# Optimization experiments

Hardware: AMD Instinct MI355X
Metric: run time of the kernel (lower is better)

The kernel has to match this reference:

```python
import jax, jax.numpy as jnp
import numpy as np

N0 = 50000
N1 = 50000
E = 500000
IN_DIM = 128
OUT_DIM = 128
H = 8
DK = OUT_DIM // H  # 16
SQRT_DK = float(np.sqrt(DK))
NUM_TYPES = 2
NUM_REL = 3
# relations: (src_type, dst_type, e_id)
RELATIONS = [(0, 1, 0), (1, 0, 1), (0, 0, 2)]


def setup_inputs() -> dict:
    key = jax.random.key(0)
    ks = jax.random.split(key, 24)
    d = {}
    d["h0"] = jax.random.normal(ks[0], (N0, IN_DIM), dtype=jnp.float32)
    d["h1"] = jax.random.normal(ks[1], (N1, IN_DIM), dtype=jnp.float32)
    d["src0"] = jax.random.randint(ks[2], (E,), 0, N0)
    d["dst0"] = jax.random.randint(ks[3], (E,), 0, N1)
    d["src1"] = jax.random.randint(ks[4], (E,), 0, N1)
    d["dst1"] = jax.random.randint(ks[5], (E,), 0, N0)
    d["src2"] = jax.random.randint(ks[6], (E,), 0, N0)
    d["dst2"] = jax.random.randint(ks[7], (E,), 0, N0)
    w_scale = 1.0 / np.sqrt(IN_DIM)
    # per-node-type stacked linear weights (k, q, v, a), torch Linear convention: y = x @ W.T + b
    d["Wk"] = jax.random.normal(ks[8], (NUM_TYPES, OUT_DIM, IN_DIM), dtype=jnp.float32) * w_scale
    d["bk"] = jnp.zeros((NUM_TYPES, OUT_DIM), dtype=jnp.float32)
    d["Wq"] = jax.random.normal(ks[9], (NUM_TYPES, OUT_DIM, IN_DIM), dtype=jnp.float32) * w_scale
    d["bq"] = jnp.zeros((NUM_TYPES, OUT_DIM), dtype=jnp.float32)
    d["Wv"] = jax.random.normal(ks[10], (NUM_TYPES, OUT_DIM, IN_DIM), dtype=jnp.float32) * w_scale
    d["bv"] = jnp.zeros((NUM_TYPES, OUT_DIM), dtype=jnp.float32)
    d["Wa"] = jax.random.normal(ks[11], (NUM_TYPES, OUT_DIM, OUT_DIM), dtype=jnp.float32) * w_scale
    d["ba"] = jnp.zeros((NUM_TYPES, OUT_DIM), dtype=jnp.float32)
    xavier = float(np.sqrt(6.0 / (DK + DK)))
    d["rel_att"] = jax.random.uniform(ks[12], (NUM_REL, H, DK, DK), dtype=jnp.float32, minval=-xavier, maxval=xavier)
    d["rel_msg"] = jax.random.uniform(ks[13], (NUM_REL, H, DK, DK), dtype=jnp.float32, minval=-xavier, maxval=xavier)
    d["rel_pri"] = jnp.ones((NUM_REL, H), dtype=jnp.float32)
    d["skip"] = jnp.ones((NUM_TYPES,), dtype=jnp.float32)
    return d


def _lin(x, W, b):
    return x @ W.T + b


def reference(h0, h1, src0, dst0, src1, dst1, src2, dst2,
              Wk, bk, Wq, bq, Wv, bv, Wa, ba,
              rel_att, rel_msg, rel_pri, skip):
    h = [h0, h1]
    edges = [(src0, dst0), (src1, dst1), (src2, dst2)]
    # per-type projections, reshaped to (N, H, DK)
    k = [_lin(h[t], Wk[t], bk[t]).reshape(-1, H, DK) for t in range(NUM_TYPES)]
    q = [_lin(h[t], Wq[t], bq[t]).reshape(-1, H, DK) for t in range(NUM_TYPES)]
    v = [_lin(h[t], Wv[t], bv[t]).reshape(-1, H, DK) for t in range(NUM_TYPES)]

    agg = [[] for _ in range(NUM_TYPES)]
    for (s, dt, e), (src, dst) in zip(RELATIONS, edges):
        # relation-specific transforms of source k and v
        kr = jnp.einsum('nhi,hij->nhj', k[s], rel_att[e])
        vr = jnp.einsum('nhi,hij->nhj', v[s], rel_msg[e])
        # per-edge dot-product score (E, H)
        score = (q[dt][dst] * kr[src]).sum(-1) * rel_pri[e] / SQRT_DK
        n_dst = h[dt].shape[0]
        # edge softmax normalized by dst (stable)
        m = jax.ops.segment_max(score, dst, num_segments=n_dst)
        ex = jnp.exp(score - m[dst])
        den = jax.ops.segment_sum(ex, dst, num_segments=n_dst)
        attn = ex / den[dst]  # (E, H)
        # weighted message scatter-sum -> (n_dst, H, DK)
        msg = vr[src] * attn[:, :, None]
        agg[dt].append(jax.ops.segment_sum(msg, dst, num_segments=n_dst))

    new_h = []
    for t in range(NUM_TYPES):
        # cross_reducer='mean' over relations targeting this node type
        tmean = sum(agg[t]) / float(len(agg[t]))
        tflat = tmean.reshape(-1, OUT_DIM)
        trans = _lin(tflat, Wa[t], ba[t])  # dropout = identity (eval)
        alpha = jax.nn.sigmoid(skip[t])
        new_h.append(trans * alpha + h[t] * (1.0 - alpha))
    return tuple(new_h)
```

## Files before the change

### kernel.cpp

```cpp
#include <hip/hip_runtime.h>

typedef __attribute__((ext_vector_type(8))) short bf16x8;
typedef __attribute__((ext_vector_type(4))) float f32x4;

#define NB 196
#define CHK 2048
#define CAPB 4096
#define PSTRIDE 6144

__device__ __forceinline__ float bflo(unsigned u) { return __uint_as_float(u << 16); }
__device__ __forceinline__ float bfhi(unsigned u) { return __uint_as_float(u & 0xFFFF0000u); }
__device__ __forceinline__ unsigned f2bf(float f) {
  unsigned u = __float_as_uint(f);
  u = (u + 0x7FFFu + ((u >> 16) & 1u)) >> 16;
  return u;
}

__global__ void cvt2_kernel(const float* __restrict__ a, unsigned short* __restrict__ oa,
                            const float* __restrict__ b, unsigned short* __restrict__ ob,
                            int n8) {
  int i = blockIdx.x * 256 + threadIdx.x;
  if (i >= n8) return;
  const float* in = blockIdx.y ? b : a;
  unsigned short* out = blockIdx.y ? ob : oa;
  const float4* p = (const float4*)(in + (size_t)i * 8);
  float4 x = p[0], y = p[1];
  uint4 v;
  v.x = f2bf(x.x) | (f2bf(x.y) << 16);
  v.y = f2bf(x.z) | (f2bf(x.w) << 16);
  v.z = f2bf(y.x) | (f2bf(y.y) << 16);
  v.w = f2bf(y.z) | (f2bf(y.w) << 16);
  *(uint4*)(out + (size_t)i * 8) = v;
}

__global__ void compose_w_kernel(const float* __restrict__ Wk, const float* __restrict__ bk,
                                 const float* __restrict__ Wv, const float* __restrict__ bv,
                                 const float* __restrict__ rel_att, const float* __restrict__ rel_msg,
                                 const float* __restrict__ rel_pri,
                                 unsigned short* __restrict__ Wkr, float* __restrict__ bkr,
                                 unsigned short* __restrict__ Wvr, float* __restrict__ bvr) {
  int e = blockIdx.x;
  int o = blockIdx.y;
  int z = blockIdx.z;
  int c = threadIdx.x;
  int hd = o >> 4, j = o & 15;
  const int se[3] = {0, 1, 0};
  int s = se[e];
  const float* W = z ? Wv : Wk;
  const float* b = z ? bv : bk;
  const float* R = z ? rel_msg : rel_att;
  float scale = z ? 1.0f : (rel_pri[e * 8 + hd] * 0.25f);
  float acc = 0.0f, bacc = 0.0f;
#pragma unroll
  for (int i = 0; i < 16; ++i) {
    float r = R[((e * 8 + hd) * 16 + i) * 16 + j];
    acc += W[(s * 128 + hd * 16 + i) * 128 + c] * r;
    bacc += b[s * 128 + hd * 16 + i] * r;
  }
  unsigned short* Wo = z ? Wvr : Wkr;
  float* bo = z ? bvr : bkr;
  Wo[((size_t)e * 128 + o) * 128 + c] = (unsigned short)f2bf(acc * scale);
  if (c == 0) bo[e * 128 + o] = bacc * scale;
}

struct ProjFP {
  const float* A[2];
  int M[2];
  int nj[2];
  const unsigned short* W[10];
  const float* b[10];
  unsigned short* out[10];
  int ostr[10];
};

__global__ __launch_bounds__(256) void proj_gemm_fused(ProjFP P) {
  __shared__ short As[128 * 128];
  __shared__ short Bs[128 * 128];
  int type = blockIdx.y;
  const float* __restrict__ A = P.A[type];
  int M = P.M[type];
  int nj = P.nj[type];
  int base = type * 5;
  int row0 = blockIdx.x * 128;
  if (row0 >= M) return;
  int t = threadIdx.x;
  bool full = (row0 + 128 <= M);
#pragma unroll
  for (int it = 0; it < 8; ++it) {
    int o = (it * 256 + t) * 8;
    int row = o >> 7, col = o & 127;
    int gr = row0 + row;
    uint4 av = make_uint4(0, 0, 0, 0);
    if (full || gr < M) {
      float4 x = *(const float4*)(A + (size_t)gr * 128 + col);
      float4 y = *(const float4*)(A + (size_t)gr * 128 + col + 4);
      av.x = f2bf(x.x) | (f2bf(x.y) << 16);
      av.y = f2bf(x.z) | (f2bf(x.w) << 16);
      av.z = f2bf(y.x) | (f2bf(y.y) << 16);
      av.w = f2bf(y.z) | (f2bf(y.w) << 16);
    }
    int sw = o ^ ((row & 7) << 3);
    *(uint4*)(&As[sw]) = av;
  }
  {
    const unsigned short* W0 = P.W[base];
#pragma unroll
    for (int it = 0; it < 8; ++it) {
      int o = (it * 256 + t) * 8;
      int row = o >> 7;
      int sw = o ^ ((row & 7) << 3);
      *(uint4*)(&Bs[sw]) = *(const uint4*)(W0 + o);
    }
  }
  __syncthreads();
  int wid = t >> 6, l = t & 63;
  int wr = wid >> 1, wc = wid & 1;
  int lr = l & 15, kb = l >> 4;
  for (int j = 0;; ++j) {
    f32x4 acc[4][4] = {};
#pragma unroll
    for (int ks = 0; ks < 4; ++ks) {
      bf16x8 af[4], bfr[4];
#pragma unroll
      for (int m = 0; m < 4; ++m) {
        int row = wr * 64 + m * 16 + lr;
        int h = (row * 128 + kb * 8 + ks * 32) ^ ((row & 7) << 3);
        af[m] = *(bf16x8*)(&As[h]);
      }
#pragma unroll
      for (int n = 0; n < 4; ++n) {
        int row = wc * 64 + n * 16 + lr;
        int h = (row * 128 + kb * 8 + ks * 32) ^ ((row & 7) << 3);
        bfr[n] = *(bf16x8*)(&Bs[h]);
      }
#pragma unroll
      for (int m = 0; m < 4; ++m)
#pragma unroll
        for (int n = 0; n < 4; ++n)
          acc[m][n] = __builtin_amdgcn_mfma_f32_16x16x32_bf16(af[m], bfr[n], acc[m][n], 0, 0, 0);
    }
    const float* bias = P.b[base + j];
    unsigned short* out = P.out[base + j];
    int ostr = P.ostr[base + j];
    int rb = row0 + wr * 64 + (l >> 4) * 4;
#pragma unroll
    for (int m = 0; m < 4; ++m)
#pragma unroll
      for (int jr = 0; jr < 4; ++jr) {
        int grow = rb + m * 16 + jr;
        if (grow < M) {
#pragma unroll
          for (int n = 0; n < 4; ++n) {
            int col = wc * 64 + n * 16 + lr;
            out[(size_t)grow * ostr + col] = (unsigned short)f2bf(acc[m][n][jr] + bias[col]);
          }
        }
      }
    if (j + 1 >= nj) break;
    __syncthreads();
    {
      const unsigned short* Wj = P.W[base + j + 1];
#pragma unroll
      for (int it = 0; it < 8; ++it) {
        int o = (it * 256 + t) * 8;
        int row = o >> 7;
        int sw = o ^ ((row & 7) << 3);
        *(uint4*)(&Bs[sw]) = *(const uint4*)(Wj + o);
      }
    }
    __syncthreads();
  }
}

__global__ __launch_bounds__(256) void final_gemm_mfma(
    float* __restrict__ dout, const unsigned short* __restrict__ Tb0,
    const unsigned short* __restrict__ Tb1, const unsigned short* __restrict__ Wab,
    const float* __restrict__ ba, const float* __restrict__ h0, const float* __restrict__ h1,
    const float* __restrict__ skip, int N0, int N1) {
  __shared__ short As[128 * 128];
  __shared__ short Bs[128 * 128];
  int type = blockIdx.y;
  int M = type ? N1 : N0;
  const unsigned short* T = type ? Tb1 : Tb0;
  const unsigned short* W = Wab + (size_t)type * 16384;
  const float* bias = ba + type * 128;
  const float* h = type ? h1 : h0;
  float* O = dout + (type ? (size_t)N0 * 128 : 0);
  int row0 = blockIdx.x * 128;
  if (row0 >= M) return;
  int t = threadIdx.x;
  bool full = (row0 + 128 <= M);
#pragma unroll
  for (int it = 0; it < 8; ++it) {
    int o = (it * 256 + t) * 8;
    int row = o >> 7;
    int gr = row0 + row;
    uint4 av = make_uint4(0, 0, 0, 0);
    if (full || gr < M) av = *(const uint4*)(T + (size_t)gr * 128 + (o & 127));
    int sw = o ^ ((row & 7) << 3);
    *(uint4*)(&As[sw]) = av;
    uint4 wv = *(const uint4*)(W + o);
    *(uint4*)(&Bs[sw]) = wv;
  }
  __syncthreads();
  int wid = t >> 6, l = t & 63;
  int wr = wid >> 1, wc = wid & 1;
  int lr = l & 15, kb = l >> 4;
  f32x4 acc[4][4] = {};
#pragma unroll
  for (int ks = 0; ks < 4; ++ks) {
    bf16x8 af[4], bfr[4];
#pragma unroll
    for (int m = 0; m < 4; ++m) {
      int row = wr * 64 + m * 16 + lr;
      int h2 = (row * 128 + kb * 8 + ks * 32) ^ ((row & 7) << 3);
      af[m] = *(bf16x8*)(&As[h2]);
    }
#pragma unroll
    for (int n = 0; n < 4; ++n) {
      int row = wc * 64 + n * 16 + lr;
      int h2 = (row * 128 + kb * 8 + ks * 32) ^ ((row & 7) << 3);
      bfr[n] = *(bf16x8*)(&Bs[h2]);
    }
#pragma unroll
    for (int m = 0; m < 4; ++m)
#pragma unroll
      for (int n = 0; n < 4; ++n)
        acc[m][n] = __builtin_amdgcn_mfma_f32_16x16x32_bf16(af[m], bfr[n], acc[m][n], 0, 0, 0);
  }
  float alpha = 1.0f / (1.0f + __expf(-skip[type]));
  float beta = 1.0f - alpha;
  int rb = row0 + wr * 64 + (l >> 4) * 4;
#pragma unroll
  for (int m = 0; m < 4; ++m)
#pragma unroll
    for (int jr = 0; jr < 4; ++jr) {
      int grow = rb + m * 16 + jr;
      if (grow < M) {
#pragma unroll
        for (int n = 0; n < 4; ++n) {
          int col = wc * 64 + n * 16 + lr;
          float vout = alpha * (acc[m][n][jr] + bias[col]) + beta * h[(size_t)grow * 128 + col];
          O[(size_t)grow * 128 + col] = vout;
        }
      }
    }
}


__global__ __launch_bounds__(256) void bhist_kernel(const int* __restrict__ d0,
                                                    const int* __restrict__ d1,
                                                    const int* __restrict__ d2,
                                                    int* __restrict__ bh, int E) {
  __shared__ int lh[NB];
  int r = blockIdx.y;
  const int* dst = r == 0 ? d0 : (r == 1 ? d1 : d2);
  int t = threadIdx.x;
  int lo = blockIdx.x * CHK;
  int hi = lo + CHK < E ? lo + CHK : E;
  for (int j = t; j < NB; j += 256) lh[j] = 0;
  __syncthreads();
  for (int i = lo + t; i < hi; i += 256) atomicAdd(&lh[dst[i] >> 8], 1);
  __syncthreads();
  for (int j = t; j < NB; j += 256) {
    int v = lh[j];
    if (v) atomicAdd(&bh[r * NB + j], v);
  }
}

__global__ void bscan_kernel(const int* __restrict__ bh, int* __restrict__ bbase, int E) {
  __shared__ int sdm[256];
  int r = blockIdx.x;
  int t = threadIdx.x;
  int v = (t < NB) ? bh[r * NB + t] : 0;
  sdm[t] = v;
  __syncthreads();
  for (int off = 1; off < 256; off <<= 1) {
    int u = (t >= off) ? sdm[t - off] : 0;
    __syncthreads();
    sdm[t] += u;
    __syncthreads();
  }
  if (t < NB) bbase[r * (NB + 1) + t] = sdm[t] - v;
  if (t == 0) bbase[r * (NB + 1) + NB] = E;
}

__global__ __launch_bounds__(256) void bin_kernel(
    const int* __restrict__ s0, const int* __restrict__ d0, const int* __restrict__ s1,
    const int* __restrict__ d1, const int* __restrict__ s2, const int* __restrict__ d2,
    const int* __restrict__ bbase, int* __restrict__ bcur, unsigned* __restrict__ bo0,
    unsigned* __restrict__ bo1, unsigned* __restrict__ bo2, int E) {
  __shared__ unsigned st[CHK];
  __shared__ int ga[CHK];
  __shared__ int hist[NB];
  __shared__ int scn[256];
  __shared__ int gb[NB];
  int r = blockIdx.y;
  const int* src = r == 0 ? s0 : (r == 1 ? s1 : s2);
  const int* dst = r == 0 ? d0 : (r == 1 ? d1 : d2);
  unsigned* bo = r == 0 ? bo0 : (r == 1 ? bo1 : bo2);
  const int* bb = bbase + r * (NB + 1);
  int t = threadIdx.x;
  int lo = blockIdx.x * CHK;
  int hi = lo + CHK < E ? lo + CHK : E;
  int nloc = hi - lo;
  if (nloc <= 0) return;
  for (int j = t; j < NB; j += 256) hist[j] = 0;
  __syncthreads();
  int myb[CHK / 256], myr[CHK / 256];
  unsigned mye[CHK / 256];
#pragma unroll
  for (int k = 0; k < CHK / 256; ++k) {
    int i = lo + k * 256 + t;
    myb[k] = -1;
    if (i < hi) {
      int d = dst[i];
      int b = d >> 8;
      mye[k] = (unsigned)src[i] | ((unsigned)d << 16);
      myb[k] = b;
      myr[k] = atomicAdd(&hist[b], 1);
    }
  }
  __syncthreads();
  int v = (t < NB) ? hist[t] : 0;
  scn[t] = v;
  __syncthreads();
  for (int off = 1; off < 256; off <<= 1) {
    int u = (t >= off) ? scn[t - off] : 0;
    __syncthreads();
    scn[t] += u;
    __syncthreads();
  }
  int excl = scn[t] - v;
  __syncthreads();
  scn[t] = excl;
  if (t < NB && v > 0) gb[t] = atomicAdd(&bcur[r * NB + t], v);
  __syncthreads();
#pragma unroll
  for (int k = 0; k < CHK / 256; ++k) {
    if (myb[k] >= 0) {
      int slot = scn[myb[k]] + myr[k];
      st[slot] = mye[k];
      ga[slot] = bb[myb[k]] + gb[myb[k]] + myr[k];
    }
  }
  __syncthreads();
  for (int j = t; j < nloc; j += 256) bo[ga[j]] = st[j];
}

__global__ __launch_bounds__(256) void bsort_kernel(
    const unsigned* __restrict__ bo0, const unsigned* __restrict__ bo1,
    const unsigned* __restrict__ bo2, const int* __restrict__ bbase, int* __restrict__ rs0,
    int* __restrict__ rs1, int* __restrict__ rs2, int* __restrict__ re0, int* __restrict__ re1,
    int* __restrict__ re2, unsigned* __restrict__ sp0, unsigned* __restrict__ sp1,
    unsigned* __restrict__ sp2, int* __restrict__ bused, int nd0, int nd1, int nd2) {
  __shared__ unsigned ed[CAPB];
  __shared__ unsigned srt[PSTRIDE];
  __shared__ unsigned short rank[CAPB];
  __shared__ int hist[256];
  __shared__ int scn[256];
  int r = blockIdx.y, b = blockIdx.x;
  const unsigned* bo = r == 0 ? bo0 : (r == 1 ? bo1 : bo2);
  int* rs = r == 0 ? rs0 : (r == 1 ? rs1 : rs2);
  int* re = r == 0 ? re0 : (r == 1 ? re1 : re2);
  unsigned* sp = r == 0 ? sp0 : (r == 1 ? sp1 : sp2);
  int nd = r == 0 ? nd0 : (r == 1 ? nd1 : nd2);
  const int* bb = bbase + r * (NB + 1);
  int base = bb[b], endb = bb[b + 1];
  int cnt = endb - base;
  if (cnt > CAPB) cnt = CAPB;
  int nlo = b << 8;
  int nn = nd - nlo;
  if (nn > 256) nn = 256;
  if (nn < 0) nn = 0;
  int t = threadIdx.x;
  hist[t] = 0;
  for (int j = t; j < cnt; j += 256) ed[j] = bo[base + j];
  __syncthreads();
  for (int j = t; j < cnt; j += 256) {
    int node = (ed[j] >> 16) & 255;
    rank[j] = (unsigned short)atomicAdd(&hist[node], 1);
  }
  __syncthreads();
  int rawh = hist[t];
  int pd = (rawh + 7) & ~7;
  scn[t] = pd;
  __syncthreads();
  for (int off = 1; off < 256; off <<= 1) {
    int u = (t >= off) ? scn[t - off] : 0;
    __syncthreads();
    scn[t] += u;
    __syncthreads();
  }
  int pexcl = scn[t] - pd;
  int ptot = scn[255];
  __syncthreads();
  hist[t] = pexcl;
  __syncthreads();
  if (t < nn) {
    rs[nlo + t] = b * PSTRIDE + pexcl;
    re[nlo + t] = b * PSTRIDE + pexcl + pd;
  }
  int ptot32 = (ptot + 31) & ~31;
  for (int j = t; j < ptot32; j += 256) srt[j] = 0xFFFFFFFFu;
  __syncthreads();
  for (int j = t; j < cnt; j += 256) {
    int node = (ed[j] >> 16) & 255;
    srt[hist[node] + rank[j]] = ed[j];
  }
  __syncthreads();
  unsigned* spb = sp + (size_t)b * PSTRIDE;
  for (int j = t; j < ptot32; j += 256) spb[j] = srt[j];
  if (t == 0) bused[r * NB + b] = ptot32;
}

struct ScP {
  const unsigned* sp[3];
  const unsigned* kv[3];
  const unsigned* qb[3];
  unsigned short* eb[3];
  const int* bused;
  int ns[3];
  int ndv[3];
};

__global__ __launch_bounds__(256) void score_kernel(ScP P) {
  int r = blockIdx.y;
  int bx = blockIdx.x;
  int bucket = bx / (PSTRIDE / 32);
  int off = (bx % (PSTRIDE / 32)) * 32;
  int used = P.bused[r * NB + bucket];
  if (off >= used) return;
  const unsigned* __restrict__ sp = P.sp[r];
  const unsigned* __restrict__ kv = P.kv[r];
  const unsigned* __restrict__ qb = P.qb[r];
  unsigned short* __restrict__ eb = P.eb[r];
  unsigned smax = (unsigned)P.ns[r] - 1;
  unsigned dmax = (unsigned)P.ndv[r] - 1;
  int t = threadIdx.x;
  int p = bucket * PSTRIDE + off + (t >> 3);
  int h = t & 7;
  unsigned pk = sp[p];
  unsigned s = pk & 0xFFFFu;
  unsigned d = pk >> 16;
  unsigned sc2 = s > smax ? smax : s;
  unsigned dc = d > dmax ? dmax : d;
  const uint4* kr = (const uint4*)((const char*)kv + ((size_t)sc2 << 9) + h * 32);
  const uint4* qr = (const uint4*)((const char*)qb + ((size_t)dc << 8) + h * 32);
  uint4 k1 = kr[0], k2 = kr[1];
  uint4 q1 = qr[0], q2 = qr[1];
  float sc = 0.f;
#pragma unroll
  for (int c = 0; c < 4; ++c) {
    unsigned ku = ((const unsigned*)&k1)[c], qu = ((const unsigned*)&q1)[c];
    sc = fmaf(bflo(ku), bflo(qu), sc);
    sc = fmaf(bfhi(ku), bfhi(qu), sc);
  }
#pragma unroll
  for (int c = 0; c < 4; ++c) {
    unsigned ku = ((const unsigned*)&k2)[c], qu = ((const unsigned*)&q2)[c];
    sc = fmaf(bflo(ku), bflo(qu), sc);
    sc = fmaf(bfhi(ku), bfhi(qu), sc);
  }
  float e = (s == 0xFFFFu) ? 0.f : __expf(sc);
  eb[(size_t)(p & ~7) * 8 + h * 8 + (p & 7)] = (unsigned short)f2bf(e);
}

struct AgP {
  const unsigned *sp0, *sp1, *sp2;
  const unsigned short *eb0, *eb1, *eb2;
  const unsigned *kv0, *kv1, *kv2;
  const int *rs0, *rs1, *rs2;
  const int *re0, *re1, *re2;
  unsigned *Tb0, *Tb1;
  int ns0, ns1, ns2;
  int N0, N1;
};

__device__ __forceinline__ void loadV(const char* __restrict__ kvl,
                                      const unsigned* __restrict__ sp,
                                      const unsigned short* __restrict__ eb, int p,
                                      unsigned smax, int half, int h, uint2 vb[4], uint2& ev) {
  unsigned sv = sp[p + (threadIdx.x & 7)];
  ev = *(const uint2*)(eb + (size_t)p * 8 + h * 8 + half * 4);
#pragma unroll
  for (int g = 0; g < 4; ++g) {
    unsigned plo = __builtin_amdgcn_readlane(sv, g);
    unsigned phi = __builtin_amdgcn_readlane(sv, g + 4);
    unsigned pk = half ? phi : plo;
    unsigned s = pk & 0xFFFFu;
    s = s > smax ? smax : s;
    vb[g] = *(const uint2*)(kvl + ((size_t)s << 9));
  }
}

__device__ __forceinline__ void computeV(const uint2 vb[4], uint2 ev, float& a0, float& a1,
                                         float& a2, float& a3, float& den) {
  float eg[4] = {bflo(ev.x), bfhi(ev.x), bflo(ev.y), bfhi(ev.y)};
#pragma unroll
  for (int g = 0; g < 4; ++g) {
    float e = eg[g];
    den += e;
    a0 = fmaf(e, bflo(vb[g].x), a0);
    a1 = fmaf(e, bfhi(vb[g].x), a1);
    a2 = fmaf(e, bflo(vb[g].y), a2);
    a3 = fmaf(e, bfhi(vb[g].y), a3);
  }
}

__device__ __forceinline__ void agg_rel(const unsigned* __restrict__ sp,
                                        const unsigned short* __restrict__ eb,
                                        const unsigned* __restrict__ kv,
                                        const int* __restrict__ rs, const int* __restrict__ re,
                                        int node, int ll, int half, unsigned smax,
                                        float& r0, float& r1, float& r2, float& r3) {
  int beg = __builtin_amdgcn_readfirstlane(rs[node]);
  int end = __builtin_amdgcn_readfirstlane(re[node]);
  if (end <= beg) return;
  int h = ll >> 2;
  const char* kvl = (const char*)kv + 256 + ll * 8;
  float a0 = 0.f, a1 = 0.f, a2 = 0.f, a3 = 0.f, den = 0.f;
  uint2 va[4], vb[4];
  uint2 ea, ebv;
  int p = beg;
  loadV(kvl, sp, eb, p, smax, half, h, va, ea);
  for (;;) {
    if (p + 8 < end) loadV(kvl, sp, eb, p + 8, smax, half, h, vb, ebv);
    computeV(va, ea, a0, a1, a2, a3, den);
    p += 8;
    if (p >= end) break;
    if (p + 8 < end) loadV(kvl, sp, eb, p + 8, smax, half, h, va, ea);
    computeV(vb, ebv, a0, a1, a2, a3, den);
    p += 8;
    if (p >= end) break;
  }
  den += __shfl_xor(den, 32);
  a0 += __shfl_xor(a0, 32);
  a1 += __shfl_xor(a1, 32);
  a2 += __shfl_xor(a2, 32);
  a3 += __shfl_xor(a3, 32);
  float inv = 1.0f / den;
  r0 = fmaf(a0, inv, r0);
  r1 = fmaf(a1, inv, r1);
  r2 = fmaf(a2, inv, r2);
  r3 = fmaf(a3, inv, r3);
}

__global__ __launch_bounds__(256) void agg2_kernel(AgP P) {
  int gw = (blockIdx.x * 256 + threadIdx.x) >> 6;
  int l = threadIdx.x & 63;
  int ll = l & 31, half = l >> 5;
  if (gw < P.N0) {
    float r0 = 0.f, r1 = 0.f, r2 = 0.f, r3 = 0.f;
    agg_rel(P.sp1, P.eb1, P.kv1, P.rs1, P.re1, gw, ll, half, (unsigned)P.ns1 - 1, r0, r1, r2, r3);
    agg_rel(P.sp2, P.eb2, P.kv2, P.rs2, P.re2, gw, ll, half, (unsigned)P.ns2 - 1, r0, r1, r2, r3);
    if (half == 0) {
      uint2 o;
      o.x = f2bf(r0 * 0.5f) | (f2bf(r1 * 0.5f) << 16);
      o.y = f2bf(r2 * 0.5f) | (f2bf(r3 * 0.5f) << 16);
      *(uint2*)(P.Tb0 + (size_t)gw * 64 + 2 * ll) = o;
    }
  } else if (gw < P.N0 + P.N1) {
    int n = gw - P.N0;
    float r0 = 0.f, r1 = 0.f, r2 = 0.f, r3 = 0.f;
    agg_rel(P.sp0, P.eb0, P.kv0, P.rs0, P.re0, n, ll, half, (unsigned)P.ns0 - 1, r0, r1, r2, r3);
    if (half == 0) {
      uint2 o;
      o.x = f2bf(r0) | (f2bf(r1) << 16);
      o.y = f2bf(r2) | (f2bf(r3) << 16);
      *(uint2*)(P.Tb1 + (size_t)n * 64 + 2 * ll) = o;
    }
  }
}

extern "C" void kernel_launch(void* const* d_in, const int* in_sizes, int n_in,
                              void* d_out, int out_size, void* d_ws, size_t ws_size,
                              hipStream_t stream) {
  const float* h0 = (const float*)d_in[0];
  const float* h1 = (const float*)d_in[1];
  const int* srcs[3] = {(const int*)d_in[2], (const int*)d_in[4], (const int*)d_in[6]};
  const int* dsts[3] = {(const int*)d_in[3], (const int*)d_in[5], (const int*)d_in[7]};
  const float* Wk = (const float*)d_in[8];
  const float* bk = (const float*)d_in[9];
  const float* Wq = (const float*)d_in[10];
  const float* bq = (const float*)d_in[11];
  const float* Wv = (const float*)d_in[12];
  const float* bv = (const float*)d_in[13];
  const float* Wa = (const float*)d_in[14];
  const float* ba = (const float*)d_in[15];
  const float* rel_att = (const float*)d_in[16];
  const float* rel_msg = (const float*)d_in[17];
  const float* rel_pri = (const float*)d_in[18];
  const float* skip = (const float*)d_in[19];

  int N0 = in_sizes[0] / 128;
  int N1 = in_sizes[1] / 128;
  int E = in_sizes[2];
  int nsrc[3] = {N0, N1, N0};
  int ndst[3] = {N1, N0, N0};
  int maxN = N0 > N1 ? N0 : N1;

  char* base = (char*)d_ws;
  size_t off = 0;
  auto alloc = [&](size_t bytes) -> void* {
    void* p = base + off;
    off += (bytes + 255) & ~(size_t)255;
    return p;
  };

  unsigned short* qb0 = (unsigned short*)alloc((size_t)N0 * 128 * 2);
  unsigned short* qb1 = (unsigned short*)alloc((size_t)N1 * 128 * 2);
  unsigned short* kvb[3];
  for (int r = 0; r < 3; ++r) kvb[r] = (unsigned short*)alloc((size_t)nsrc[r] * 256 * 2);
  unsigned short* Tb0 = (unsigned short*)alloc((size_t)N0 * 128 * 2);
  unsigned short* Tb1 = (unsigned short*)alloc((size_t)N1 * 128 * 2);
  unsigned short* Wkrb = (unsigned short*)alloc((size_t)3 * 16384 * 2);
  unsigned short* Wvrb = (unsigned short*)alloc((size_t)3 * 16384 * 2);
  unsigned short* Wqb = (unsigned short*)alloc((size_t)2 * 16384 * 2);
  unsigned short* Wab = (unsigned short*)alloc((size_t)2 * 16384 * 2);
  float* bkr = (float*)alloc(3 * 128 * 4);
  float* bvr = (float*)alloc(3 * 128 * 4);
  int* rp_s[3];
  int* rp_e[3];
  unsigned* spk[3];
  unsigned short* eb[3];
  unsigned* bo[3];
  for (int r = 0; r < 3; ++r) {
    rp_s[r] = (int*)alloc((size_t)ndst[r] * 4);
    rp_e[r] = (int*)alloc((size_t)ndst[r] * 4);
    spk[r] = (unsigned*)alloc((size_t)NB * PSTRIDE * 4);
    eb[r] = (unsigned short*)alloc((size_t)NB * PSTRIDE * 8 * 2);
    bo[r] = (unsigned*)alloc((size_t)(E + 8) * 4);
  }
  int* bcnt = (int*)alloc((size_t)2 * 3 * NB * 4);
  int* bhist = bcnt;
  int* bcur = bcnt + 3 * NB;
  int* bbase = (int*)alloc((size_t)3 * (NB + 1) * 4);
  int* bused = (int*)alloc((size_t)3 * NB * 4);
  (void)ws_size;

  compose_w_kernel<<<dim3(3, 128, 2), 128, 0, stream>>>(Wk, bk, Wv, bv, rel_att, rel_msg,
                                                        rel_pri, Wkrb, bkr, Wvrb, bvr);
  cvt2_kernel<<<dim3(16, 2), 256, 0, stream>>>(Wq, Wqb, Wa, Wab, 4096);

  ProjFP pf;
  pf.A[0] = h0; pf.A[1] = h1;
  pf.M[0] = N0; pf.M[1] = N1;
  pf.nj[0] = 5; pf.nj[1] = 3;
  pf.W[0] = Wqb;            pf.b[0] = bq;        pf.out[0] = qb0;          pf.ostr[0] = 128;
  pf.W[1] = Wkrb;           pf.b[1] = bkr;       pf.out[1] = kvb[0];       pf.ostr[1] = 256;
  pf.W[2] = Wkrb + 32768;   pf.b[2] = bkr + 256; pf.out[2] = kvb[2];       pf.ostr[2] = 256;
  pf.W[3] = Wvrb;           pf.b[3] = bvr;       pf.out[3] = kvb[0] + 128; pf.ostr[3] = 256;
  pf.W[4] = Wvrb + 32768;   pf.b[4] = bvr + 256; pf.out[4] = kvb[2] + 128; pf.ostr[4] = 256;
  pf.W[5] = Wqb + 16384;    pf.b[5] = bq + 128;  pf.out[5] = qb1;          pf.ostr[5] = 128;
  pf.W[6] = Wkrb + 16384;   pf.b[6] = bkr + 128; pf.out[6] = kvb[1];       pf.ostr[6] = 256;
  pf.W[7] = Wvrb + 16384;   pf.b[7] = bvr + 128; pf.out[7] = kvb[1] + 128; pf.ostr[7] = 256;
  pf.W[8] = Wqb; pf.b[8] = bq; pf.out[8] = qb0; pf.ostr[8] = 128;
  pf.W[9] = Wqb; pf.b[9] = bq; pf.out[9] = qb0; pf.ostr[9] = 128;
  proj_gemm_fused<<<dim3((maxN + 127) / 128, 2), 256, 0, stream>>>(pf);

  hipMemsetAsync(bcnt, 0, (size_t)2 * 3 * NB * 4, stream);
  bhist_kernel<<<dim3((E + CHK - 1) / CHK, 3), 256, 0, stream>>>(dsts[0], dsts[1], dsts[2],
                                                                 bhist, E);
  bscan_kernel<<<3, 256, 0, stream>>>(bhist, bbase, E);
  bin_kernel<<<dim3((E + CHK - 1) / CHK, 3), 256, 0, stream>>>(
      srcs[0], dsts[0], srcs[1], dsts[1], srcs[2], dsts[2], bbase, bcur, bo[0], bo[1], bo[2], E);
  bsort_kernel<<<dim3(NB, 3), 256, 0, stream>>>(
      bo[0], bo[1], bo[2], bbase, rp_s[0], rp_s[1], rp_s[2], rp_e[0], rp_e[1], rp_e[2],
      spk[0], spk[1], spk[2], bused, ndst[0], ndst[1], ndst[2]);

  ScP sp;
  for (int r = 0; r < 3; ++r) {
    sp.sp[r] = spk[r];
    sp.kv[r] = (const unsigned*)kvb[r];
    sp.eb[r] = eb[r];
    sp.ns[r] = nsrc[r];
    sp.ndv[r] = ndst[r];
  }
  sp.bused = bused;
  sp.qb[0] = (const unsigned*)qb1;
  sp.qb[1] = (const unsigned*)qb0;
  sp.qb[2] = (const unsigned*)qb0;
  score_kernel<<<dim3(NB * (PSTRIDE / 32), 3), 256, 0, stream>>>(sp);

  AgP ap;
  ap.sp0 = spk[0]; ap.sp1 = spk[1]; ap.sp2 = spk[2];
  ap.eb0 = eb[0]; ap.eb1 = eb[1]; ap.eb2 = eb[2];
  ap.kv0 = (const unsigned*)kvb[0]; ap.kv1 = (const unsigned*)kvb[1];
  ap.kv2 = (const unsigned*)kvb[2];
  ap.rs0 = rp_s[0]; ap.rs1 = rp_s[1]; ap.rs2 = rp_s[2];
  ap.re0 = rp_e[0]; ap.re1 = rp_e[1]; ap.re2 = rp_e[2];
  ap.ns0 = nsrc[0]; ap.ns1 = nsrc[1]; ap.ns2 = nsrc[2];
  ap.Tb0 = (unsigned*)Tb0; ap.Tb1 = (unsigned*)Tb1;
  ap.N0 = N0; ap.N1 = N1;
  int totw = N0 + N1;
  agg2_kernel<<<(totw + 3) / 4, 256, 0, stream>>>(ap);

  final_gemm_mfma<<<dim3((maxN + 127) / 128, 2), 256, 0, stream>>>(
      (float*)d_out, Tb0, Tb1, Wab, ba, h0, h1, skip, N0, N1);
}
```

Before: 263.4 us.

## Fuse edge score computation into aggregation kernel, dropping score buffer

Removes the separate score kernel and its bf16 exp-score buffer. The aggregation kernel now loads each destination's q once, gathers k and v rows per edge, computes the per-head dot product with DPP lane reductions, and applies exp inline. Padded slots point to a zeroed sentinel row whose exp(0)=1 contributions are subtracted from the denominator using the raw count now stored in the row-end array. This saves one launch and a write/read of the score array, at the cost of double gather width per edge in the aggregation loop and extra DPP/exp work per lane.

```diff
diff --git a/kernel.cpp b/kernel.cpp
--- a/kernel.cpp
+++ b/kernel.cpp
@@ -15,6 +15,9 @@
   u = (u + 0x7FFFu + ((u >> 16) & 1u)) >> 16;
   return u;
 }
+
+#define DPPADD(v, ctrl) \
+  ((v) + __int_as_float(__builtin_amdgcn_update_dpp(0, __float_as_int(v), ctrl, 0xF, 0xF, true)))
 
 __global__ void cvt2_kernel(const float* __restrict__ a, unsigned short* __restrict__ oa,
                             const float* __restrict__ b, unsigned short* __restrict__ ob,
@@ -353,7 +356,7 @@
     const unsigned* __restrict__ bo2, const int* __restrict__ bbase, int* __restrict__ rs0,
     int* __restrict__ rs1, int* __restrict__ rs2, int* __restrict__ re0, int* __restrict__ re1,
     int* __restrict__ re2, unsigned* __restrict__ sp0, unsigned* __restrict__ sp1,
-    unsigned* __restrict__ sp2, int* __restrict__ bused, int nd0, int nd1, int nd2) {
+    unsigned* __restrict__ sp2, int nd0, int nd1, int nd2, int ns0, int ns1, int ns2) {
   __shared__ unsigned ed[CAPB];
   __shared__ unsigned srt[PSTRIDE];
   __shared__ unsigned short rank[CAPB];
@@ -365,6 +368,7 @@
   int* re = r == 0 ? re0 : (r == 1 ? re1 : re2);
   unsigned* sp = r == 0 ? sp0 : (r == 1 ? sp1 : sp2);
   int nd = r == 0 ? nd0 : (r == 1 ? nd1 : nd2);
+  unsigned sentinel = (unsigned)(r == 0 ? ns0 : (r == 1 ? ns1 : ns2));
   const int* bb = bbase + r * (NB + 1);
   int base = bb[b], endb = bb[b + 1];
   int cnt = endb - base;
@@ -399,10 +403,10 @@
   __syncthreads();
   if (t < nn) {
     rs[nlo + t] = b * PSTRIDE + pexcl;
-    re[nlo + t] = b * PSTRIDE + pexcl + pd;
+    re[nlo + t] = b * PSTRIDE + pexcl + rawh;
   }
   int ptot32 = (ptot + 31) & ~31;
-  for (int j = t; j < ptot32; j += 256) srt[j] = 0xFFFFFFFFu;
+  for (int j = t; j < ptot32; j += 256) srt[j] = sentinel;
   __syncthreads();
   for (int j = t; j < cnt; j += 256) {
     int node = (ed[j] >> 16) & 255;
@@ -411,126 +415,76 @@
   __syncthreads();
   unsigned* spb = sp + (size_t)b * PSTRIDE;
   for (int j = t; j < ptot32; j += 256) spb[j] = srt[j];
-  if (t == 0) bused[r * NB + b] = ptot32;
-}
-
-struct ScP {
-  const unsigned* sp[3];
-  const unsigned* kv[3];
-  const unsigned* qb[3];
-  unsigned short* eb[3];
-  const int* bused;
-  int ns[3];
-  int ndv[3];
-};
-
-__global__ __launch_bounds__(256) void score_kernel(ScP P) {
-  int r = blockIdx.y;
-  int bx = blockIdx.x;
-  int bucket = bx / (PSTRIDE / 32);
-  int off = (bx % (PSTRIDE / 32)) * 32;
-  int used = P.bused[r * NB + bucket];
-  if (off >= used) return;
-  const unsigned* __restrict__ sp = P.sp[r];
-  const unsigned* __restrict__ kv = P.kv[r];
-  const unsigned* __restrict__ qb = P.qb[r];
-  unsigned short* __restrict__ eb = P.eb[r];
-  unsigned smax = (unsigned)P.ns[r] - 1;
-  unsigned dmax = (unsigned)P.ndv[r] - 1;
-  int t = threadIdx.x;
-  int p = bucket * PSTRIDE + off + (t >> 3);
-  int h = t & 7;
-  unsigned pk = sp[p];
-  unsigned s = pk & 0xFFFFu;
-  unsigned d = pk >> 16;
-  unsigned sc2 = s > smax ? smax : s;
-  unsigned dc = d > dmax ? dmax : d;
-  const uint4* kr = (const uint4*)((const char*)kv + ((size_t)sc2 << 9) + h * 32);
-  const uint4* qr = (const uint4*)((const char*)qb + ((size_t)dc << 8) + h * 32);
-  uint4 k1 = kr[0], k2 = kr[1];
-  uint4 q1 = qr[0], q2 = qr[1];
-  float sc = 0.f;
-#pragma unroll
-  for (int c = 0; c < 4; ++c) {
-    unsigned ku = ((const unsigned*)&k1)[c], qu = ((const unsigned*)&q1)[c];
-    sc = fmaf(bflo(ku), bflo(qu), sc);
-    sc = fmaf(bfhi(ku), bfhi(qu), sc);
-  }
-#pragma unroll
-  for (int c = 0; c < 4; ++c) {
-    unsigned ku = ((const unsigned*)&k2)[c], qu = ((const unsigned*)&q2)[c];
-    sc = fmaf(bflo(ku), bflo(qu), sc);
-    sc = fmaf(bfhi(ku), bfhi(qu), sc);
-  }
-  float e = (s == 0xFFFFu) ? 0.f : __expf(sc);
-  eb[(size_t)(p & ~7) * 8 + h * 8 + (p & 7)] = (unsigned short)f2bf(e);
-}
-
-struct AgP {
+}
+
+struct FuP {
   const unsigned *sp0, *sp1, *sp2;
-  const unsigned short *eb0, *eb1, *eb2;
   const unsigned *kv0, *kv1, *kv2;
+  const unsigned *qb0, *qb1;
   const int *rs0, *rs1, *rs2;
   const int *re0, *re1, *re2;
   unsigned *Tb0, *Tb1;
-  int ns0, ns1, ns2;
   int N0, N1;
 };
 
-__device__ __forceinline__ void loadV(const char* __restrict__ kvl,
-                                      const unsigned* __restrict__ sp,
-                                      const unsigned short* __restrict__ eb, int p,
-                                      unsigned smax, int half, int h, uint2 vb[4], uint2& ev) {
+__device__ __forceinline__ void loadKV(const char* __restrict__ kvl,
+                                       const unsigned* __restrict__ sp, int p, int half,
+                                       uint2 kf[4], uint2 vf[4]) {
   unsigned sv = sp[p + (threadIdx.x & 7)];
-  ev = *(const uint2*)(eb + (size_t)p * 8 + h * 8 + half * 4);
 #pragma unroll
   for (int g = 0; g < 4; ++g) {
-    unsigned plo = __builtin_amdgcn_readlane(sv, g);
-    unsigned phi = __builtin_amdgcn_readlane(sv, g + 4);
-    unsigned pk = half ? phi : plo;
-    unsigned s = pk & 0xFFFFu;
-    s = s > smax ? smax : s;
-    vb[g] = *(const uint2*)(kvl + ((size_t)s << 9));
-  }
-}
-
-__device__ __forceinline__ void computeV(const uint2 vb[4], uint2 ev, float& a0, float& a1,
-                                         float& a2, float& a3, float& den) {
-  float eg[4] = {bflo(ev.x), bfhi(ev.x), bflo(ev.y), bfhi(ev.y)};
+    unsigned pA = __builtin_amdgcn_readlane(sv, g);
+    unsigned pB = __builtin_amdgcn_readlane(sv, g + 4);
+    unsigned pk = half ? pB : pA;
+    const char* row = kvl + ((size_t)(pk & 0xFFFFu) << 9);
+    kf[g] = *(const uint2*)row;
+    vf[g] = *(const uint2*)(row + 256);
+  }
+}
+
+__device__ __forceinline__ void computeKV(const uint2 kf[4], const uint2 vf[4], float qx0,
+                                          float qy0, float qx1, float qy1, float& a0, float& a1,
+                                          float& a2, float& a3, float& den) {
 #pragma unroll
   for (int g = 0; g < 4; ++g) {
-    float e = eg[g];
+    float sc = qx0 * bflo(kf[g].x) + qy0 * bfhi(kf[g].x) + qx1 * bflo(kf[g].y) +
+               qy1 * bfhi(kf[g].y);
+    sc = DPPADD(sc, 0xB1);
+    sc = DPPADD(sc, 0x4E);
+    float e = __expf(sc);
     den += e;
-    a0 = fmaf(e, bflo(vb[g].x), a0);
-    a1 = fmaf(e, bfhi(vb[g].x), a1);
-    a2 = fmaf(e, bflo(vb[g].y), a2);
-    a3 = fmaf(e, bfhi(vb[g].y), a3);
-  }
-}
-
-__device__ __forceinline__ void agg_rel(const unsigned* __restrict__ sp,
-                                        const unsigned short* __restrict__ eb,
-                                        const unsigned* __restrict__ kv,
-                                        const int* __restrict__ rs, const int* __restrict__ re,
-                                        int node, int ll, int half, unsigned smax,
-                                        float& r0, float& r1, float& r2, float& r3) {
+    a0 = fmaf(e, bflo(vf[g].x), a0);
+    a1 = fmaf(e, bfhi(vf[g].x), a1);
+    a2 = fmaf(e, bflo(vf[g].y), a2);
+    a3 = fmaf(e, bfhi(vf[g].y), a3);
+  }
+}
+
+__device__ __forceinline__ void fuse_rel(const unsigned* __restrict__ sp,
+                                         const unsigned* __restrict__ kv,
+                                         const int* __restrict__ rs, const int* __restrict__ re,
+                                         int node, int ll, int half, float qx0, float qy0,
+                                         float qx1, float qy1, float& r0, float& r1, float& r2,
+                                         float& r3) {
   int beg = __builtin_amdgcn_readfirstlane(rs[node]);
-  int end = __builtin_amdgcn_readfirstlane(re[node]);
-  if (end <= beg) return;
-  int h = ll >> 2;
-  const char* kvl = (const char*)kv + 256 + ll * 8;
+  int rend = __builtin_amdgcn_readfirstlane(re[node]);
+  int raw = rend - beg;
+  if (raw <= 0) return;
+  int pd = (raw + 7) & ~7;
+  int end = beg + pd;
+  float npad = (float)(pd - raw);
+  const char* kvl = (const char*)kv + ll * 8;
   float a0 = 0.f, a1 = 0.f, a2 = 0.f, a3 = 0.f, den = 0.f;
-  uint2 va[4], vb[4];
-  uint2 ea, ebv;
+  uint2 ka[4], va[4], kb2[4], vb2[4];
   int p = beg;
-  loadV(kvl, sp, eb, p, smax, half, h, va, ea);
+  loadKV(kvl, sp, p, half, ka, va);
   for (;;) {
-    if (p + 8 < end) loadV(kvl, sp, eb, p + 8, smax, half, h, vb, ebv);
-    computeV(va, ea, a0, a1, a2, a3, den);
+    if (p + 8 < end) loadKV(kvl, sp, p + 8, half, kb2, vb2);
+    computeKV(ka, va, qx0, qy0, qx1, qy1, a0, a1, a2, a3, den);
     p += 8;
     if (p >= end) break;
-    if (p + 8 < end) loadV(kvl, sp, eb, p + 8, smax, half, h, va, ea);
-    computeV(vb, ebv, a0, a1, a2, a3, den);
+    if (p + 8 < end) loadKV(kvl, sp, p + 8, half, ka, va);
+    computeKV(kb2, vb2, qx0, qy0, qx1, qy1, a0, a1, a2, a3, den);
     p += 8;
     if (p >= end) break;
   }
@@ -539,6 +493,7 @@
   a1 += __shfl_xor(a1, 32);
   a2 += __shfl_xor(a2, 32);
   a3 += __shfl_xor(a3, 32);
+  den -= npad;
   float inv = 1.0f / den;
   r0 = fmaf(a0, inv, r0);
   r1 = fmaf(a1, inv, r1);
@@ -546,14 +501,16 @@
   r3 = fmaf(a3, inv, r3);
 }
 
-__global__ __launch_bounds__(256) void agg2_kernel(AgP P) {
+__global__ __launch_bounds__(256) void fusedge_kernel(FuP P) {
   int gw = (blockIdx.x * 256 + threadIdx.x) >> 6;
   int l = threadIdx.x & 63;
   int ll = l & 31, half = l >> 5;
   if (gw < P.N0) {
+    uint2 q = *(const uint2*)((const char*)P.qb0 + (size_t)gw * 256 + ll * 8);
+    float qx0 = bflo(q.x), qy0 = bfhi(q.x), qx1 = bflo(q.y), qy1 = bfhi(q.y);
     float r0 = 0.f, r1 = 0.f, r2 = 0.f, r3 = 0.f;
-    agg_rel(P.sp1, P.eb1, P.kv1, P.rs1, P.re1, gw, ll, half, (unsigned)P.ns1 - 1, r0, r1, r2, r3);
-    agg_rel(P.sp2, P.eb2, P.kv2, P.rs2, P.re2, gw, ll, half, (unsigned)P.ns2 - 1, r0, r1, r2, r3);
+    fuse_rel(P.sp1, P.kv1, P.rs1, P.re1, gw, ll, half, qx0, qy0, qx1, qy1, r0, r1, r2, r3);
+    fuse_rel(P.sp2, P.kv2, P.rs2, P.re2, gw, ll, half, qx0, qy0, qx1, qy1, r0, r1, r2, r3);
     if (half == 0) {
       uint2 o;
       o.x = f2bf(r0 * 0.5f) | (f2bf(r1 * 0.5f) << 16);
@@ -562,8 +519,10 @@
     }
   } else if (gw < P.N0 + P.N1) {
     int n = gw - P.N0;
+    uint2 q = *(const uint2*)((const char*)P.qb1 + (size_t)n * 256 + ll * 8);
+    float qx0 = bflo(q.x), qy0 = bfhi(q.x), qx1 = bflo(q.y), qy1 = bfhi(q.y);
     float r0 = 0.f, r1 = 0.f, r2 = 0.f, r3 = 0.f;
-    agg_rel(P.sp0, P.eb0, P.kv0, P.rs0, P.re0, n, ll, half, (unsigned)P.ns0 - 1, r0, r1, r2, r3);
+    fuse_rel(P.sp0, P.kv0, P.rs0, P.re0, n, ll, half, qx0, qy0, qx1, qy1, r0, r1, r2, r3);
     if (half == 0) {
       uint2 o;
       o.x = f2bf(r0) | (f2bf(r1) << 16);
@@ -611,7 +570,7 @@
   unsigned short* qb0 = (unsigned short*)alloc((size_t)N0 * 128 * 2);
   unsigned short* qb1 = (unsigned short*)alloc((size_t)N1 * 128 * 2);
   unsigned short* kvb[3];
-  for (int r = 0; r < 3; ++r) kvb[r] = (unsigned short*)alloc((size_t)nsrc[r] * 256 * 2);
+  for (int r = 0; r < 3; ++r) kvb[r] = (unsigned short*)alloc((size_t)(nsrc[r] + 1) * 256 * 2);
   unsigned short* Tb0 = (unsigned short*)alloc((size_t)N0 * 128 * 2);
   unsigned short* Tb1 = (unsigned short*)alloc((size_t)N1 * 128 * 2);
   unsigned short* Wkrb = (unsigned short*)alloc((size_t)3 * 16384 * 2);
@@ -623,21 +582,21 @@
   int* rp_s[3];
   int* rp_e[3];
   unsigned* spk[3];
-  unsigned short* eb[3];
   unsigned* bo[3];
   for (int r = 0; r < 3; ++r) {
     rp_s[r] = (int*)alloc((size_t)ndst[r] * 4);
     rp_e[r] = (int*)alloc((size_t)ndst[r] * 4);
     spk[r] = (unsigned*)alloc((size_t)NB * PSTRIDE * 4);
-    eb[r] = (unsigned short*)alloc((size_t)NB * PSTRIDE * 8 * 2);
     bo[r] = (unsigned*)alloc((size_t)(E + 8) * 4);
   }
   int* bcnt = (int*)alloc((size_t)2 * 3 * NB * 4);
   int* bhist = bcnt;
   int* bcur = bcnt + 3 * NB;
   int* bbase = (int*)alloc((size_t)3 * (NB + 1) * 4);
-  int* bused = (int*)alloc((size_t)3 * NB * 4);
   (void)ws_size;
+
+  for (int r = 0; r < 3; ++r)
+    hipMemsetAsync(kvb[r] + (size_t)nsrc[r] * 256, 0, 512, stream);
 
   compose_w_kernel<<<dim3(3, 128, 2), 128, 0, stream>>>(Wk, bk, Wv, bv, rel_att, rel_msg,
                                                         rel_pri, Wkrb, bkr, Wvrb, bvr);
@@ -667,34 +626,19 @@
       srcs[0], dsts[0], srcs[1], dsts[1], srcs[2], dsts[2], bbase, bcur, bo[0], bo[1], bo[2], E);
   bsort_kernel<<<dim3(NB, 3), 256, 0, stream>>>(
       bo[0], bo[1], bo[2], bbase, rp_s[0], rp_s[1], rp_s[2], rp_e[0], rp_e[1], rp_e[2],
-      spk[0], spk[1], spk[2], bused, ndst[0], ndst[1], ndst[2]);
-
-  ScP sp;
-  for (int r = 0; r < 3; ++r) {
-    sp.sp[r] = spk[r];
-    sp.kv[r] = (const unsigned*)kvb[r];
-    sp.eb[r] = eb[r];
-    sp.ns[r] = nsrc[r];
-    sp.ndv[r] = ndst[r];
-  }
-  sp.bused = bused;
-  sp.qb[0] = (const unsigned*)qb1;
-  sp.qb[1] = (const unsigned*)qb0;
-  sp.qb[2] = (const unsigned*)qb0;
-  score_kernel<<<dim3(NB * (PSTRIDE / 32), 3), 256, 0, stream>>>(sp);
-
-  AgP ap;
-  ap.sp0 = spk[0]; ap.sp1 = spk[1]; ap.sp2 = spk[2];
-  ap.eb0 = eb[0]; ap.eb1 = eb[1]; ap.eb2 = eb[2];
-  ap.kv0 = (const unsigned*)kvb[0]; ap.kv1 = (const unsigned*)kvb[1];
-  ap.kv2 = (const unsigned*)kvb[2];
-  ap.rs0 = rp_s[0]; ap.rs1 = rp_s[1]; ap.rs2 = rp_s[2];
-  ap.re0 = rp_e[0]; ap.re1 = rp_e[1]; ap.re2 = rp_e[2];
-  ap.ns0 = nsrc[0]; ap.ns1 = nsrc[1]; ap.ns2 = nsrc[2];
-  ap.Tb0 = (unsigned*)Tb0; ap.Tb1 = (unsigned*)Tb1;
-  ap.N0 = N0; ap.N1 = N1;
+      spk[0], spk[1], spk[2], ndst[0], ndst[1], ndst[2], nsrc[0], nsrc[1], nsrc[2]);
+
+  FuP fp2;
+  fp2.sp0 = spk[0]; fp2.sp1 = spk[1]; fp2.sp2 = spk[2];
+  fp2.kv0 = (const unsigned*)kvb[0]; fp2.kv1 = (const unsigned*)kvb[1];
+  fp2.kv2 = (const unsigned*)kvb[2];
+  fp2.qb0 = (const unsigned*)qb0; fp2.qb1 = (const unsigned*)qb1;
+  fp2.rs0 = rp_s[0]; fp2.rs1 = rp_s[1]; fp2.rs2 = rp_s[2];
+  fp2.re0 = rp_e[0]; fp2.re1 = rp_e[1]; fp2.re2 = rp_e[2];
+  fp2.Tb0 = (unsigned*)Tb0; fp2.Tb1 = (unsigned*)Tb1;
+  fp2.N0 = N0; fp2.N1 = N1;
   int totw = N0 + N1;
-  agg2_kernel<<<(totw + 3) / 4, 256, 0, stream>>>(ap);
+  fusedge_kernel<<<(totw + 3) / 4, 256, 0, stream>>>(fp2);
 
   final_gemm_mfma<<<dim3((maxN + 127) / 128, 2), 256, 0, stream>>>(
       (float*)d_out, Tb0, Tb1, Wab, ba, h0, h1, skip, N0, N1);
```

After: 243.7 us. 7.5% less time.
